# Kernel tuning notes

Hardware: AMD Instinct MI355X
Metric: run time of the kernel (lower is better)

## Reference

```python
import jax, jax.numpy as jnp
import numpy as np

B, T, H, A, E, V = 32, 128, 1024, 1024, 512, 512  # A==H required by the module's cat/Linear shapes


def setup_inputs() -> dict:
    key = jax.random.key(0)
    ks = jax.random.split(key, 13)
    s = 0.02
    return {
        "encoder_outputs": jax.random.normal(ks[0], (B, A, E), jnp.float32),
        "hidden": jax.random.normal(ks[1], (1, B, H), jnp.float32),
        "target_seq": jax.random.normal(ks[2], (B, T, H), jnp.float32),
        "W_att": jax.random.normal(ks[3], (H + A, A), jnp.float32) * s,
        "b_att": jax.random.normal(ks[4], (A,), jnp.float32) * s,
        "W_comb": jax.random.normal(ks[5], (H + E, H), jnp.float32) * s,
        "b_comb": jax.random.normal(ks[6], (H,), jnp.float32) * s,
        "W_ih": jax.random.normal(ks[7], (3 * H, H), jnp.float32) * s,
        "b_ih": jax.random.normal(ks[8], (3 * H,), jnp.float32) * s,
        "W_hh": jax.random.normal(ks[9], (3 * H, H), jnp.float32) * s,
        "b_hh": jax.random.normal(ks[10], (3 * H,), jnp.float32) * s,
        "W_out": jax.random.normal(ks[11], (H, V), jnp.float32) * s,
        "b_out": jax.random.normal(ks[12], (V,), jnp.float32) * s,
    }


def reference(encoder_outputs, hidden, target_seq, W_att, b_att, W_comb, b_comb,
              W_ih, b_ih, W_hh, b_hh, W_out, b_out):
    # Teacher forcing: decoder input at step t is zeros (t=0) then target_seq[:, t-1]
    dec_in = jnp.concatenate([jnp.zeros_like(target_seq[:, :1]), target_seq[:, :-1]], axis=1)  # [B,T,H]
    dec_ts = jnp.swapaxes(dec_in, 0, 1)  # [T,B,H]

    def step(h, dec):  # h: [B,H], dec: [B,H]
        # attention over encoder positions (softmax width A == encoder seq len)
        attn = jax.nn.softmax(jnp.concatenate([dec, h], axis=1) @ W_att + b_att, axis=1)  # [B,A]
        ctx = jnp.einsum('bl,ble->be', attn, encoder_outputs)  # [B,E]
        g = jax.nn.relu(jnp.concatenate([dec, ctx], axis=1) @ W_comb + b_comb)  # [B,H]
        # GRU cell (torch gate order r, z, n)
        gi = g @ W_ih.T + b_ih
        gh = h @ W_hh.T + b_hh
        ir, iz, i_n = jnp.split(gi, 3, axis=1)
        hr, hz, h_n = jnp.split(gh, 3, axis=1)
        r = jax.nn.sigmoid(ir + hr)
        z = jax.nn.sigmoid(iz + hz)
        n = jnp.tanh(i_n + r * h_n)
        h_new = (1.0 - z) * n + z * h
        out_tok = h_new @ W_out + b_out  # [B,V]
        return h_new, out_tok

    h_last, outs = jax.lax.scan(step, hidden[0], dec_ts)  # outs: [T,B,V]
    output_seq = jnp.swapaxes(outs, 0, 1)  # [B,T,V]
    return output_seq, h_last[None]
```

## Files before the change

kernel.cpp:

```cpp
#include <hip/hip_runtime.h>

typedef unsigned short u16;
typedef unsigned int u32;
typedef unsigned long long u64;
typedef short v8s __attribute__((ext_vector_type(8)));
typedef float v4f __attribute__((ext_vector_type(4)));

#define MFMA16(a, b, c) __builtin_amdgcn_mfma_f32_16x16x32_bf16((a), (b), (c), 0, 0, 0)

#define B_ 32
#define T_ 128
#define H_ 1024
#define A_ 1024
#define E_ 512
#define V_ 512
#define NBLK 256
#define NTH 512
#define NSLOT 32
#define ENC_LDS_BYTES 131072
#define SCRATCH_BYTES 28672
#define DSMEM_BYTES (ENC_LDS_BYTES + SCRATCH_BYTES)

__device__ __forceinline__ float b2f(u16 u) {
  union { u32 u; float f; } c; c.u = ((u32)u) << 16; return c.f;
}
__device__ __forceinline__ u16 f2b(float f) {
  union { float f; u32 u; } c; c.f = f;
  u32 x = c.u;
  x += 0x7fffu + ((x >> 16) & 1u);
  return (u16)(x >> 16);
}

__device__ __forceinline__ u32 ato_ld(const u32* p) {
  return __hip_atomic_load(p, __ATOMIC_RELAXED, __HIP_MEMORY_SCOPE_AGENT);
}
__device__ __forceinline__ void ato_st(u32* p, u32 v) {
  __hip_atomic_store(p, v, __ATOMIC_RELAXED, __HIP_MEMORY_SCOPE_AGENT);
}
__device__ __forceinline__ float ato_ldf(const float* p) {
  union { u32 u; float f; } c; c.u = ato_ld((const u32*)p); return c.f;
}
__device__ __forceinline__ void ato_stf(float* p, float v) {
  union { float f; u32 u; } c; c.f = v; ato_st((u32*)p, c.u);
}
__device__ __forceinline__ v8s ld_frag(const u16* p) {
  u64 a = __hip_atomic_load((const u64*)p, __ATOMIC_RELAXED, __HIP_MEMORY_SCOPE_AGENT);
  u64 b = __hip_atomic_load((const u64*)(p + 4), __ATOMIC_RELAXED, __HIP_MEMORY_SCOPE_AGENT);
  union { u64 q[2]; v8s v; } u; u.q[0] = a; u.q[1] = b; return u.v;
}

__device__ __forceinline__ void grid_bar(u32* arr, u32 ep) {
  asm volatile("s_waitcnt vmcnt(0)" ::: "memory");
  __syncthreads();
  u32* gen = arr + NBLK * NSLOT;
  if (blockIdx.x == 0) {
    int i = threadIdx.x;
    if (i >= 1 && i < NBLK) {
      while (__hip_atomic_load(arr + i * NSLOT, __ATOMIC_RELAXED, __HIP_MEMORY_SCOPE_AGENT) < ep)
        __builtin_amdgcn_s_sleep(1);
    }
    __syncthreads();
    if (threadIdx.x == 0)
      __hip_atomic_store(gen, ep, __ATOMIC_RELAXED, __HIP_MEMORY_SCOPE_AGENT);
  } else {
    if (threadIdx.x == 0) {
      __hip_atomic_store(arr + blockIdx.x * NSLOT, ep, __ATOMIC_RELAXED, __HIP_MEMORY_SCOPE_AGENT);
      while (__hip_atomic_load(gen, __ATOMIC_RELAXED, __HIP_MEMORY_SCOPE_AGENT) < ep)
        __builtin_amdgcn_s_sleep(1);
    }
    __syncthreads();
  }
  asm volatile("" ::: "memory");
}

__device__ __forceinline__ void gemm_nk(const u16* ah, const u16* al, size_t mstr,
                                        const u16* bp, int nk, v4f& c0, v4f& c1) {
  #pragma unroll 2
  for (int i = 0; i < nk; ++i) {
    v8s b   = *(const v8s*)(bp);
    v8s a0h = *(const v8s*)(ah);
    v8s a1h = *(const v8s*)(ah + mstr);
    v8s a0l = *(const v8s*)(al);
    v8s a1l = *(const v8s*)(al + mstr);
    c0 = MFMA16(a0h, b, c0);
    c1 = MFMA16(a1h, b, c1);
    c0 = MFMA16(a0l, b, c0);
    c1 = MFMA16(a1l, b, c1);
    ah += 32; al += 32; bp += 32;
  }
}
__device__ __forceinline__ void gemm_nk_a(const u16* ah, const u16* al, size_t mstr,
                                          const u16* bp, int nk, v4f& c0, v4f& c1) {
  #pragma unroll 2
  for (int i = 0; i < nk; ++i) {
    v8s b   = *(const v8s*)(bp);
    v8s a0h = ld_frag(ah);
    v8s a1h = ld_frag(ah + mstr);
    v8s a0l = ld_frag(al);
    v8s a1l = ld_frag(al + mstr);
    c0 = MFMA16(a0h, b, c0);
    c1 = MFMA16(a1h, b, c1);
    c0 = MFMA16(a0l, b, c0);
    c1 = MFMA16(a1l, b, c1);
    ah += 32; al += 32; bp += 32;
  }
}

__device__ __forceinline__ void red_store2(float* part, int wv, int lane, v4f c0, v4f c1) {
  float* p = part + (wv * 64 + lane) * 8;
  #pragma unroll
  for (int r = 0; r < 4; ++r) { p[r] = c0[r]; p[4 + r] = c1[r]; }
}
__device__ __forceinline__ float red_sum2(const float* part, int o) {
  int m = o >> 4, n = o & 15;
  int lane = (((m & 15) >> 2) << 4) + n;
  int idx = ((m >> 4) << 2) + (m & 3);
  float s = 0.f;
  #pragma unroll
  for (int w = 0; w < 8; ++w) s += part[(w * 64 + lane) * 8 + idx];
  return s;
}

__global__ void __launch_bounds__(NTH, 1)
dec_persist(const u16* __restrict__ tgt_hi, const u16* __restrict__ tgt_lo,
            const u16* __restrict__ WattT, const u16* __restrict__ Whh_b,
            const u16* __restrict__ Wih_b, const u16* __restrict__ WcombT,
            const float* __restrict__ enc_f,
            const float* __restrict__ batt, const float* __restrict__ bcomb,
            const float* __restrict__ bih, const float* __restrict__ bhh,
            float* h, float* logit, float* gh, float* g_dec, float* logit_dec,
            u16* ctx_hi, u16* ctx_lo, u16* g_hi, u16* g_lo,
            u16* hbf_hi, u16* hbf_lo, u16* hseqb, u32* bar)
{
  const int tid = threadIdx.x;
  const int bid = blockIdx.x;
  const int lane = tid & 63;
  const int wv = tid >> 6;
  const int ln = lane & 15;
  const int kq8 = (lane >> 4) * 8;

  extern __shared__ __align__(16) unsigned char dsm[];
  u16* lds_enc = (u16*)dsm;
  float* scratch = (float*)(dsm + ENC_LDS_BYTES);

  {
    int b = bid >> 3, e0 = (bid & 7) * 64;
    const float* src = enc_f + (size_t)b * A_ * E_ + e0 + (tid & 7) * 8;
    int seg = (tid & 7) * 8;
    for (int i = 0; i < 16; ++i) {
      int row = i * 64 + (tid >> 3);
      const float* sp = src + (size_t)row * E_;
      float4 a = *(const float4*)sp;
      float4 bq = *(const float4*)(sp + 4);
      u16 tmp[8] = {f2b(a.x), f2b(a.y), f2b(a.z), f2b(a.w),
                    f2b(bq.x), f2b(bq.y), f2b(bq.z), f2b(bq.w)};
      *(v8s*)(lds_enc + row * 64 + seg) = *(v8s*)tmp;
    }
  }

  u32 ep = 0;

  for (int t = 0; t < T_; ++t) {
    {
      float* part = scratch;
      int u = bid;
      v4f c0 = {0.f, 0.f, 0.f, 0.f}, c1 = {0.f, 0.f, 0.f, 0.f};
      if (u < 64) {
        int n0 = u * 16;
        const u16* bp = WattT + (size_t)(n0 + ln) * 2048 + 1024 + wv * 128 + kq8;
        size_t abase = (size_t)ln * H_ + wv * 128 + kq8;
        gemm_nk_a(hbf_hi + abase, hbf_lo + abase, (size_t)16 * H_, bp, 4, c0, c1);
      } else {
        int j0 = (u - 64) * 16;
        const u16* bp = Whh_b + (size_t)(j0 + ln) * H_ + wv * 128 + kq8;
        size_t abase = (size_t)ln * H_ + wv * 128 + kq8;
        gemm_nk_a(hbf_hi + abase, hbf_lo + abase, (size_t)16 * H_, bp, 4, c0, c1);
      }
      red_store2(part, wv, lane, c0, c1);
      __syncthreads();
      {
        float s = red_sum2(part, tid);
        int m = tid >> 4, n = tid & 15;
        if (u < 64) {
          int n0 = u * 16;
          float v = s + ato_ldf(&logit_dec[(t & 1) * (B_ * A_) + m * A_ + n0 + n])
                  + batt[n0 + n];
          ato_stf(&logit[m * A_ + n0 + n], v);
        } else {
          int j0 = (u - 64) * 16;
          ato_stf(&gh[(size_t)(j0 + n) * 32 + m], s + bhh[j0 + n]);
        }
      }
    }
    grid_bar(bar, ++ep);

    {
      float* p    = scratch;
      float* part = scratch + 1024;
      float* red  = scratch + 5120;
      float* sctx = scratch + 5136;
      int b = bid >> 3, e0 = (bid & 7) * 64;
      float v1 = ato_ldf(&logit[b * A_ + tid]);
      float v2 = ato_ldf(&logit[b * A_ + 512 + tid]);
      float mx = fmaxf(v1, v2);
      #pragma unroll
      for (int off = 32; off; off >>= 1) mx = fmaxf(mx, __shfl_xor(mx, off));
      if (lane == 0) red[wv] = mx;
      __syncthreads();
      float mfull = red[0];
      #pragma unroll
      for (int q = 1; q < 8; ++q) mfull = fmaxf(mfull, red[q]);
      float e1 = __expf(v1 - mfull), e2 = __expf(v2 - mfull);
      p[tid] = e1; p[512 + tid] = e2;
      float sm = e1 + e2;
      #pragma unroll
      for (int off = 32; off; off >>= 1) sm += __shfl_xor(sm, off);
      if (lane == 0) red[8 + wv] = sm;
      __syncthreads();
      float ssum = red[8];
      #pragma unroll
      for (int q = 1; q < 8; ++q) ssum += red[8 + q];
      float inv = 1.f / ssum;

      int le = lane & 7, lr = lane >> 3;
      float acc[8] = {0.f, 0.f, 0.f, 0.f, 0.f, 0.f, 0.f, 0.f};
      #pragma unroll 4
      for (int i = 0; i < 16; ++i) {
        int l = i * 64 + wv * 8 + lr;
        v8s w = *(const v8s*)(lds_enc + l * 64 + le * 8);
        float pv = p[l];
        #pragma unroll
        for (int r = 0; r < 8; ++r) acc[r] += pv * b2f((u16)w[r]);
      }
      float* pp = part + ((wv * 8 + lr) * 8 + le) * 8;
      #pragma unroll
      for (int r = 0; r < 8; ++r) pp[r] = acc[r];
      __syncthreads();
      if (tid < 64) {
        int eo = tid >> 3, r = tid & 7;
        float s = 0.f;
        #pragma unroll
        for (int q = 0; q < 64; ++q) s += part[q * 64 + eo * 8 + r];
        sctx[tid] = s * inv;
      }
      __syncthreads();
      if (tid < 32) {
        float s0 = sctx[2 * tid], s1 = sctx[2 * tid + 1];
        u16 h0 = f2b(s0), h1 = f2b(s1);
        u16 l0 = f2b(s0 - b2f(h0)), l1 = f2b(s1 - b2f(h1));
        int idx = b * E_ + e0 + 2 * tid;
        ato_st((u32*)(ctx_hi + idx), (u32)h0 | ((u32)h1 << 16));
        ato_st((u32*)(ctx_lo + idx), (u32)l0 | ((u32)l1 << 16));
      }
    }
    grid_bar(bar, ++ep);

    {
      if (bid < 64) {
        float* part = scratch;
        int n0 = bid * 16;
        v4f c0 = {0.f, 0.f, 0.f, 0.f}, c1 = {0.f, 0.f, 0.f, 0.f};
        const u16* bp = WcombT + (size_t)(n0 + ln) * 1536 + 1024 + wv * 64 + kq8;
        size_t abase = (size_t)ln * E_ + wv * 64 + kq8;
        gemm_nk_a(ctx_hi + abase, ctx_lo + abase, (size_t)16 * E_, bp, 2, c0, c1);
        red_store2(part, wv, lane, c0, c1);
        __syncthreads();
        int m = tid >> 4, n = tid & 15;
        float s = red_sum2(part, tid) + ato_ldf(&g_dec[(t & 1) * (B_ * H_) + m * H_ + n0 + n])
                + bcomb[n0 + n];
        s = fmaxf(s, 0.f);
        __syncthreads();
        float* gx = part;
        gx[m * 16 + n] = s;
        __syncthreads();
        if (tid < 256) {
          int m2 = tid >> 3, n2 = (tid & 7) * 2;
          float s0 = gx[m2 * 16 + n2], s1 = gx[m2 * 16 + n2 + 1];
          u16 h0 = f2b(s0), h1 = f2b(s1);
          u16 l0 = f2b(s0 - b2f(h0)), l1 = f2b(s1 - b2f(h1));
          int idx = m2 * H_ + n0 + n2;
          ato_st((u32*)(g_hi + idx), (u32)h0 | ((u32)h1 << 16));
          ato_st((u32*)(g_lo + idx), (u32)l0 | ((u32)l1 << 16));
        }
      }
    }
    grid_bar(bar, ++ep);

    {
      if (bid < 64) {
        float* part = scratch;
        float* hx   = scratch + 6144;
        int j0 = bid * 16;
        v4f c00 = {0.f,0.f,0.f,0.f}, c01 = c00, c02 = c00, c10 = c00, c11 = c00, c12 = c00;
        size_t abase = (size_t)ln * H_ + wv * 128 + kq8;
        const u16* ah = g_hi + abase;
        const u16* al = g_lo + abase;
        const u16* bp0 = Wih_b + (size_t)(j0 + ln) * H_ + wv * 128 + kq8;
        const u16* bp1 = bp0 + (size_t)H_ * H_;
        const u16* bp2 = bp0 + (size_t)2 * H_ * H_;
        #pragma unroll
        for (int i = 0; i < 4; ++i) {
          v8s b0 = *(const v8s*)bp0, b1 = *(const v8s*)bp1, b2 = *(const v8s*)bp2;
          v8s a0h = ld_frag(ah), a0l = ld_frag(al);
          v8s a1h = ld_frag(ah + 16 * H_), a1l = ld_frag(al + 16 * H_);
          c00 = MFMA16(a0h, b0, c00); c00 = MFMA16(a0l, b0, c00);
          c01 = MFMA16(a0h, b1, c01); c01 = MFMA16(a0l, b1, c01);
          c02 = MFMA16(a0h, b2, c02); c02 = MFMA16(a0l, b2, c02);
          c10 = MFMA16(a1h, b0, c10); c10 = MFMA16(a1l, b0, c10);
          c11 = MFMA16(a1h, b1, c11); c11 = MFMA16(a1l, b1, c11);
          c12 = MFMA16(a1h, b2, c12); c12 = MFMA16(a1l, b2, c12);
          ah += 32; al += 32; bp0 += 32; bp1 += 32; bp2 += 32;
        }
        #pragma unroll
        for (int pass = 0; pass < 2; ++pass) {
          float* pp = part + (wv * 64 + lane) * 12;
          if (pass == 0) {
            #pragma unroll
            for (int r = 0; r < 4; ++r) { pp[r] = c00[r]; pp[4 + r] = c01[r]; pp[8 + r] = c02[r]; }
          } else {
            #pragma unroll
            for (int r = 0; r < 4; ++r) { pp[r] = c10[r]; pp[4 + r] = c11[r]; pp[8 + r] = c12[r]; }
          }
          __syncthreads();
          if (tid < 256) {
            int obl = tid >> 4, jj = tid & 15;
            int ob = pass * 16 + obl;
            int j = j0 + jj;
            int lanei = ((obl >> 2) << 4) + jj;
            int rg = obl & 3;
            float ir = 0.f, iz = 0.f, in_ = 0.f;
            #pragma unroll
            for (int w = 0; w < 8; ++w) {
              const float* q = part + (w * 64 + lanei) * 12;
              ir += q[rg]; iz += q[4 + rg]; in_ += q[8 + rg];
            }
            ir += bih[j]; iz += bih[H_ + j]; in_ += bih[2 * H_ + j];
            float hr = ato_ldf(&gh[(size_t)j * 32 + ob]);
            float hz = ato_ldf(&gh[(size_t)(H_ + j) * 32 + ob]);
            float hn = ato_ldf(&gh[(size_t)(2 * H_ + j) * 32 + ob]);
            float r = 1.f / (1.f + __expf(-(ir + hr)));
            float z = 1.f / (1.f + __expf(-(iz + hz)));
            float n = tanhf(in_ + r * hn);
            float ho = h[ob * H_ + j];
            float hnew = (1.f - z) * n + z * ho;
            h[ob * H_ + j] = hnew;
            hx[ob * 16 + jj] = hnew;
          }
          __syncthreads();
        }
        if (tid < 256) {
          int ob2 = tid >> 3, j2 = (tid & 7) * 2;
          float v0 = hx[ob2 * 16 + j2], v1 = hx[ob2 * 16 + j2 + 1];
          u16 h0 = f2b(v0), h1 = f2b(v1);
          u16 l0 = f2b(v0 - b2f(h0)), l1 = f2b(v1 - b2f(h1));
          int idx = ob2 * H_ + j0 + j2;
          u32 hp = (u32)h0 | ((u32)h1 << 16);
          ato_st((u32*)(hbf_hi + idx), hp);
          ato_st((u32*)(hbf_lo + idx), (u32)l0 | ((u32)l1 << 16));
          *(u32*)(hseqb + ((size_t)t * 32 + ob2) * H_ + j0 + j2) = hp;
        }
      } else if (bid < 128) {
        if (t < T_ - 1) {
          float* part = scratch;
          int n0 = (bid - 64) * 16;
          v4f c0 = {0.f, 0.f, 0.f, 0.f}, c1 = {0.f, 0.f, 0.f, 0.f};
          size_t abase = ((size_t)ln * T_ + t) * H_ + wv * 128 + kq8;
          const u16* bp = WattT + (size_t)(n0 + ln) * 2048 + wv * 128 + kq8;
          gemm_nk(tgt_hi + abase, tgt_lo + abase, (size_t)16 * T_ * H_, bp, 4, c0, c1);
          red_store2(part, wv, lane, c0, c1);
          __syncthreads();
          int m = tid >> 4, n = tid & 15;
          ato_stf(&logit_dec[((t + 1) & 1) * (B_ * A_) + m * A_ + n0 + n], red_sum2(part, tid));
        }
      } else if (bid < 192) {
        if (t < T_ - 1) {
          float* part = scratch;
          int n0 = (bid - 128) * 16;
          v4f c0 = {0.f, 0.f, 0.f, 0.f}, c1 = {0.f, 0.f, 0.f, 0.f};
          size_t abase = ((size_t)ln * T_ + t) * H_ + wv * 128 + kq8;
          const u16* bp = WcombT + (size_t)(n0 + ln) * 1536 + wv * 128 + kq8;
          gemm_nk(tgt_hi + abase, tgt_lo + abase, (size_t)16 * T_ * H_, bp, 4, c0, c1);
          red_store2(part, wv, lane, c0, c1);
          __syncthreads();
          int m = tid >> 4, n = tid & 15;
          ato_stf(&g_dec[((t + 1) & 1) * (B_ * H_) + m * H_ + n0 + n], red_sum2(part, tid));
        }
      }
    }
    grid_bar(bar, ++ep);
  }
}

__global__ void __launch_bounds__(256, 2)
out_gemm(const u16* __restrict__ hseqb, const u16* __restrict__ WoutT,
         const float* __restrict__ bout, float* __restrict__ out)
{
  int tid = threadIdx.x, lane = tid & 63, wv = tid >> 6;
  int ln = lane & 15, kq8 = (lane >> 4) * 8;
  int m0 = (blockIdx.x >> 3) * 32;
  int n0 = (blockIdx.x & 7) * 64 + wv * 16;
  v4f c0 = {0.f, 0.f, 0.f, 0.f}, c1 = {0.f, 0.f, 0.f, 0.f};
  const u16* ap = hseqb + (size_t)(m0 + ln) * 1024 + kq8;
  const u16* bp = WoutT + (size_t)(n0 + ln) * 1024 + kq8;
  for (int i = 0; i < 32; ++i) {
    v8s b = *(const v8s*)bp;
    v8s a0 = *(const v8s*)ap;
    v8s a1 = *(const v8s*)(ap + 16 * 1024);
    c0 = MFMA16(a0, b, c0);
    c1 = MFMA16(a1, b, c1);
    ap += 32; bp += 32;
  }
  int v = n0 + ln;
  float bo = bout[v];
  int rbase = (lane >> 4) * 4;
  #pragma unroll
  for (int rg = 0; rg < 4; ++rg) {
    int m = m0 + rbase + rg;
    out[((size_t)(m & 31) * T_ + (m >> 5)) * V_ + v] = c0[rg] + bo;
    int m2 = m + 16;
    out[((size_t)(m2 & 31) * T_ + (m2 >> 5)) * V_ + v] = c1[rg] + bo;
  }
}

__global__ void __launch_bounds__(256)
hlast_copy(const float* __restrict__ h, float* __restrict__ out)
{
  int i = blockIdx.x * 256 + threadIdx.x;
  if (i < B_ * H_) out[(size_t)B_ * T_ * V_ + i] = h[i];
}

__global__ void __launch_bounds__(256)
k_cvt(const float* __restrict__ in, u16* __restrict__ out, int n)
{
  int stride = gridDim.x * 256;
  for (int i = blockIdx.x * 256 + threadIdx.x; i < n; i += stride) out[i] = f2b(in[i]);
}

__global__ void __launch_bounds__(256)
k_cvt_split(const float* __restrict__ in, u16* __restrict__ hi, u16* __restrict__ lo, int n)
{
  int stride = gridDim.x * 256;
  for (int i = blockIdx.x * 256 + threadIdx.x; i < n; i += stride) {
    float x = in[i];
    u16 a = f2b(x);
    hi[i] = a;
    lo[i] = f2b(x - b2f(a));
  }
}

__global__ void __launch_bounds__(256)
k_tr(const float* __restrict__ in, u16* __restrict__ out, int R, int C)
{
  __shared__ float tile[32][33];
  int tc = C >> 5;
  int r0 = (blockIdx.x / tc) << 5, c0 = (blockIdx.x % tc) << 5;
  int tx = threadIdx.x & 31, ty = threadIdx.x >> 5;
  #pragma unroll
  for (int q = 0; q < 4; ++q) {
    int r = ty + q * 8;
    tile[r][tx] = in[(size_t)(r0 + r) * C + c0 + tx];
  }
  __syncthreads();
  #pragma unroll
  for (int q = 0; q < 4; ++q) {
    int r = ty + q * 8;
    out[(size_t)(c0 + r) * R + r0 + tx] = f2b(tile[tx][r]);
  }
}

__global__ void __launch_bounds__(256)
k_init(const float* __restrict__ hidden, float* h, u16* hhi, u16* hlo)
{
  int i = blockIdx.x * 256 + threadIdx.x;
  if (i < B_ * H_) {
    float x = hidden[i];
    h[i] = x;
    u16 a = f2b(x);
    hhi[i] = a;
    hlo[i] = f2b(x - b2f(a));
  }
}

extern "C" void kernel_launch(void* const* d_in, const int* in_sizes, int n_in,
                              void* d_out, int out_size, void* d_ws, size_t ws_size,
                              hipStream_t stream) {
  (void)in_sizes; (void)n_in; (void)out_size; (void)ws_size;
  const float* enc    = (const float*)d_in[0];
  const float* hidden = (const float*)d_in[1];
  const float* tgt    = (const float*)d_in[2];
  const float* Watt   = (const float*)d_in[3];
  const float* batt   = (const float*)d_in[4];
  const float* Wcomb  = (const float*)d_in[5];
  const float* bcomb  = (const float*)d_in[6];
  const float* Wih    = (const float*)d_in[7];
  const float* bih    = (const float*)d_in[8];
  const float* Whh    = (const float*)d_in[9];
  const float* bhh    = (const float*)d_in[10];
  const float* Wout   = (const float*)d_in[11];
  const float* bout   = (const float*)d_in[12];

  size_t off = 0;
  char* base = (char*)d_ws;
  auto alloc = [&](size_t bytes) -> void* {
    void* p = base + off;
    off += (bytes + 255) & ~(size_t)255;
    return p;
  };
  size_t bar_bytes = (size_t)(NBLK * NSLOT + NSLOT) * 4;
  u32*   bar    = (u32*)  alloc(bar_bytes);
  float* h      = (float*)alloc(B_ * H_ * 4);
  float* logit  = (float*)alloc(B_ * A_ * 4);
  float* gh     = (float*)alloc((size_t)3 * H_ * B_ * 4);
  float* g_dec  = (float*)alloc((size_t)2 * B_ * H_ * 4);
  float* logit_dec = (float*)alloc((size_t)2 * B_ * A_ * 4);
  u16*   ctx_hi = (u16*)  alloc(B_ * E_ * 2);
  u16*   ctx_lo = (u16*)  alloc(B_ * E_ * 2);
  u16*   g_hi   = (u16*)  alloc(B_ * H_ * 2);
  u16*   g_lo   = (u16*)  alloc(B_ * H_ * 2);
  u16*   hbf_hi = (u16*)  alloc(B_ * H_ * 2);
  u16*   hbf_lo = (u16*)  alloc(B_ * H_ * 2);
  u16*   hseqb  = (u16*)  alloc((size_t)T_ * B_ * H_ * 2);
  u16*   tgt_hi = (u16*)  alloc((size_t)B_ * T_ * H_ * 2);
  u16*   tgt_lo = (u16*)  alloc((size_t)B_ * T_ * H_ * 2);
  u16*   WattT  = (u16*)  alloc((size_t)2048 * 1024 * 2);
  u16*   Whh_b  = (u16*)  alloc((size_t)3 * H_ * H_ * 2);
  u16*   Wih_b  = (u16*)  alloc((size_t)3 * H_ * H_ * 2);
  u16*   WcombT = (u16*)  alloc((size_t)1024 * 1536 * 2);
  u16*   WoutT  = (u16*)  alloc((size_t)512 * 1024 * 2);

  hipMemsetAsync(bar, 0, bar_bytes, stream);
  hipMemsetAsync(g_dec, 0, (size_t)2 * B_ * H_ * 4, stream);
  hipMemsetAsync(logit_dec, 0, (size_t)2 * B_ * A_ * 4, stream);

  k_cvt_split<<<2048, 256, 0, stream>>>(tgt, tgt_hi, tgt_lo, B_ * T_ * H_);
  k_cvt<<<2048, 256, 0, stream>>>(Whh, Whh_b, 3 * H_ * H_);
  k_cvt<<<2048, 256, 0, stream>>>(Wih, Wih_b, 3 * H_ * H_);
  k_tr<<<64 * 32, 256, 0, stream>>>(Watt, WattT, 2048, 1024);
  k_tr<<<48 * 32, 256, 0, stream>>>(Wcomb, WcombT, 1536, 1024);
  k_tr<<<32 * 16, 256, 0, stream>>>(Wout, WoutT, 1024, 512);
  k_init<<<128, 256, 0, stream>>>(hidden, h, hbf_hi, hbf_lo);

  hipFuncSetAttribute((const void*)dec_persist,
                      hipFuncAttributeMaxDynamicSharedMemorySize, DSMEM_BYTES);

  dec_persist<<<NBLK, NTH, DSMEM_BYTES, stream>>>(tgt_hi, tgt_lo, WattT, Whh_b, Wih_b, WcombT,
                                                  enc, batt, bcomb, bih, bhh,
                                                  h, logit, gh, g_dec, logit_dec,
                                                  ctx_hi, ctx_lo, g_hi, g_lo,
                                                  hbf_hi, hbf_lo, hseqb, bar);
  out_gemm<<<1024, 256, 0, stream>>>(hseqb, WoutT, bout, (float*)d_out);
  hlast_copy<<<128, 256, 0, stream>>>(h, (float*)d_out);
}
```

Before: 4.524 ms.

## Fuse ctx-to-comb projection into attention phase via atomic accumulation, drop a grid barrier

Each attention block now multiplies its 64-element context slice by the matching rows of the ctx part of W_comb and atomically adds the partial result into a float g accumulator. The separate comb GEMM phase and its grid barrier are removed, so there is one fewer global synchronization per timestep. The GRU input phase applies bias and ReLU and does the bf16 hi/lo split on the fly when loading g. The cost is fp32 atomics to global memory with nondeterministic summation order, extra zeroing stores for the double buffer, and a CUDA-core dot product in place of MFMA.

```diff
diff --git a/kernel.cpp b/kernel.cpp
--- a/kernel.cpp
+++ b/kernel.cpp
@@ -43,10 +43,30 @@
 __device__ __forceinline__ void ato_stf(float* p, float v) {
   union { float f; u32 u; } c; c.f = v; ato_st((u32*)p, c.u);
 }
+__device__ __forceinline__ void ato_addf(float* p, float v) {
+  __hip_atomic_fetch_add(p, v, __ATOMIC_RELAXED, __HIP_MEMORY_SCOPE_AGENT);
+}
 __device__ __forceinline__ v8s ld_frag(const u16* p) {
   u64 a = __hip_atomic_load((const u64*)p, __ATOMIC_RELAXED, __HIP_MEMORY_SCOPE_AGENT);
   u64 b = __hip_atomic_load((const u64*)(p + 4), __ATOMIC_RELAXED, __HIP_MEMORY_SCOPE_AGENT);
   union { u64 q[2]; v8s v; } u; u.q[0] = a; u.q[1] = b; return u.v;
+}
+__device__ __forceinline__ void ld_g8(const float* gp, const float* bc, v8s& hi, v8s& lo) {
+  float v[8];
+  #pragma unroll
+  for (int i = 0; i < 8; i += 2) {
+    u64 q = __hip_atomic_load((const u64*)(gp + i), __ATOMIC_RELAXED, __HIP_MEMORY_SCOPE_AGENT);
+    union { u64 q; float f[2]; } c; c.q = q;
+    v[i] = c.f[0]; v[i + 1] = c.f[1];
+  }
+  u16 hh[8], ll[8];
+  #pragma unroll
+  for (int i = 0; i < 8; ++i) {
+    float x = fmaxf(v[i] + bc[i], 0.f);
+    u16 a = f2b(x);
+    hh[i] = a; ll[i] = f2b(x - b2f(a));
+  }
+  hi = *(v8s*)hh; lo = *(v8s*)ll;
 }
 
 __device__ __forceinline__ void grid_bar(u32* arr, u32 ep) {
@@ -125,11 +145,11 @@
 dec_persist(const u16* __restrict__ tgt_hi, const u16* __restrict__ tgt_lo,
             const u16* __restrict__ WattT, const u16* __restrict__ Whh_b,
             const u16* __restrict__ Wih_b, const u16* __restrict__ WcombT,
+            const u16* __restrict__ Wc_ctx,
             const float* __restrict__ enc_f,
             const float* __restrict__ batt, const float* __restrict__ bcomb,
             const float* __restrict__ bih, const float* __restrict__ bhh,
-            float* h, float* logit, float* gh, float* g_dec, float* logit_dec,
-            u16* ctx_hi, u16* ctx_lo, u16* g_hi, u16* g_lo,
+            float* h, float* logit, float* gh, float* g_acc, float* logit_dec,
             u16* hbf_hi, u16* hbf_lo, u16* hseqb, u32* bar)
 {
   const int tid = threadIdx.x;
@@ -163,15 +183,15 @@
   for (int t = 0; t < T_; ++t) {
     {
       float* part = scratch;
-      int u = bid;
       v4f c0 = {0.f, 0.f, 0.f, 0.f}, c1 = {0.f, 0.f, 0.f, 0.f};
-      if (u < 64) {
-        int n0 = u * 16;
+      if (bid < 64) {
+        ato_stf(&g_acc[((t + 1) & 1) * (B_ * H_) + bid * 512 + tid], 0.f);
+        int n0 = bid * 16;
         const u16* bp = WattT + (size_t)(n0 + ln) * 2048 + 1024 + wv * 128 + kq8;
         size_t abase = (size_t)ln * H_ + wv * 128 + kq8;
         gemm_nk_a(hbf_hi + abase, hbf_lo + abase, (size_t)16 * H_, bp, 4, c0, c1);
       } else {
-        int j0 = (u - 64) * 16;
+        int j0 = (bid - 64) * 16;
         const u16* bp = Whh_b + (size_t)(j0 + ln) * H_ + wv * 128 + kq8;
         size_t abase = (size_t)ln * H_ + wv * 128 + kq8;
         gemm_nk_a(hbf_hi + abase, hbf_lo + abase, (size_t)16 * H_, bp, 4, c0, c1);
@@ -181,13 +201,13 @@
       {
         float s = red_sum2(part, tid);
         int m = tid >> 4, n = tid & 15;
-        if (u < 64) {
-          int n0 = u * 16;
+        if (bid < 64) {
+          int n0 = bid * 16;
           float v = s + ato_ldf(&logit_dec[(t & 1) * (B_ * A_) + m * A_ + n0 + n])
                   + batt[n0 + n];
           ato_stf(&logit[m * A_ + n0 + n], v);
         } else {
-          int j0 = (u - 64) * 16;
+          int j0 = (bid - 64) * 16;
           ato_stf(&gh[(size_t)(j0 + n) * 32 + m], s + bhh[j0 + n]);
         }
       }
@@ -199,7 +219,7 @@
       float* part = scratch + 1024;
       float* red  = scratch + 5120;
       float* sctx = scratch + 5136;
-      int b = bid >> 3, e0 = (bid & 7) * 64;
+      int b = bid >> 3, es = bid & 7;
       float v1 = ato_ldf(&logit[b * A_ + tid]);
       float v2 = ato_ldf(&logit[b * A_ + 512 + tid]);
       float mx = fmaxf(v1, v2);
@@ -244,44 +264,19 @@
         sctx[tid] = s * inv;
       }
       __syncthreads();
-      if (tid < 32) {
-        float s0 = sctx[2 * tid], s1 = sctx[2 * tid + 1];
-        u16 h0 = f2b(s0), h1 = f2b(s1);
-        u16 l0 = f2b(s0 - b2f(h0)), l1 = f2b(s1 - b2f(h1));
-        int idx = b * E_ + e0 + 2 * tid;
-        ato_st((u32*)(ctx_hi + idx), (u32)h0 | ((u32)h1 << 16));
-        ato_st((u32*)(ctx_lo + idx), (u32)l0 | ((u32)l1 << 16));
-      }
-    }
-    grid_bar(bar, ++ep);
-
-    {
-      if (bid < 64) {
-        float* part = scratch;
-        int n0 = bid * 16;
-        v4f c0 = {0.f, 0.f, 0.f, 0.f}, c1 = {0.f, 0.f, 0.f, 0.f};
-        const u16* bp = WcombT + (size_t)(n0 + ln) * 1536 + 1024 + wv * 64 + kq8;
-        size_t abase = (size_t)ln * E_ + wv * 64 + kq8;
-        gemm_nk_a(ctx_hi + abase, ctx_lo + abase, (size_t)16 * E_, bp, 2, c0, c1);
-        red_store2(part, wv, lane, c0, c1);
-        __syncthreads();
-        int m = tid >> 4, n = tid & 15;
-        float s = red_sum2(part, tid) + ato_ldf(&g_dec[(t & 1) * (B_ * H_) + m * H_ + n0 + n])
-                + bcomb[n0 + n];
-        s = fmaxf(s, 0.f);
-        __syncthreads();
-        float* gx = part;
-        gx[m * 16 + n] = s;
-        __syncthreads();
-        if (tid < 256) {
-          int m2 = tid >> 3, n2 = (tid & 7) * 2;
-          float s0 = gx[m2 * 16 + n2], s1 = gx[m2 * 16 + n2 + 1];
-          u16 h0 = f2b(s0), h1 = f2b(s1);
-          u16 l0 = f2b(s0 - b2f(h0)), l1 = f2b(s1 - b2f(h1));
-          int idx = m2 * H_ + n0 + n2;
-          ato_st((u32*)(g_hi + idx), (u32)h0 | ((u32)h1 << 16));
-          ato_st((u32*)(g_lo + idx), (u32)l0 | ((u32)l1 << 16));
-        }
+      {
+        const u16* wrow = Wc_ctx + (size_t)(es * 64) * H_ + tid * 2;
+        float a0 = 0.f, a1 = 0.f;
+        #pragma unroll 4
+        for (int e = 0; e < 64; ++e) {
+          u32 w = *(const u32*)(wrow + (size_t)e * H_);
+          float pv = sctx[e];
+          a0 += pv * b2f((u16)w);
+          a1 += pv * b2f((u16)(w >> 16));
+        }
+        float* gp = g_acc + (t & 1) * (B_ * H_) + b * H_ + tid * 2;
+        ato_addf(gp, a0);
+        ato_addf(gp + 1, a1);
       }
     }
     grid_bar(bar, ++ep);
@@ -292,24 +287,24 @@
         float* hx   = scratch + 6144;
         int j0 = bid * 16;
         v4f c00 = {0.f,0.f,0.f,0.f}, c01 = c00, c02 = c00, c10 = c00, c11 = c00, c12 = c00;
-        size_t abase = (size_t)ln * H_ + wv * 128 + kq8;
-        const u16* ah = g_hi + abase;
-        const u16* al = g_lo + abase;
-        const u16* bp0 = Wih_b + (size_t)(j0 + ln) * H_ + wv * 128 + kq8;
+        const float* gbase = g_acc + (t & 1) * (B_ * H_);
+        int koff = wv * 128 + kq8;
+        const u16* bp0 = Wih_b + (size_t)(j0 + ln) * H_ + koff;
         const u16* bp1 = bp0 + (size_t)H_ * H_;
         const u16* bp2 = bp0 + (size_t)2 * H_ * H_;
         #pragma unroll
         for (int i = 0; i < 4; ++i) {
           v8s b0 = *(const v8s*)bp0, b1 = *(const v8s*)bp1, b2 = *(const v8s*)bp2;
-          v8s a0h = ld_frag(ah), a0l = ld_frag(al);
-          v8s a1h = ld_frag(ah + 16 * H_), a1l = ld_frag(al + 16 * H_);
+          v8s a0h, a0l, a1h, a1l;
+          ld_g8(gbase + (size_t)ln * H_ + koff, bcomb + koff, a0h, a0l);
+          ld_g8(gbase + (size_t)(ln + 16) * H_ + koff, bcomb + koff, a1h, a1l);
           c00 = MFMA16(a0h, b0, c00); c00 = MFMA16(a0l, b0, c00);
           c01 = MFMA16(a0h, b1, c01); c01 = MFMA16(a0l, b1, c01);
           c02 = MFMA16(a0h, b2, c02); c02 = MFMA16(a0l, b2, c02);
           c10 = MFMA16(a1h, b0, c10); c10 = MFMA16(a1l, b0, c10);
           c11 = MFMA16(a1h, b1, c11); c11 = MFMA16(a1l, b1, c11);
           c12 = MFMA16(a1h, b2, c12); c12 = MFMA16(a1l, b2, c12);
-          ah += 32; al += 32; bp0 += 32; bp1 += 32; bp2 += 32;
+          koff += 32; bp0 += 32; bp1 += 32; bp2 += 32;
         }
         #pragma unroll
         for (int pass = 0; pass < 2; ++pass) {
@@ -383,7 +378,7 @@
           red_store2(part, wv, lane, c0, c1);
           __syncthreads();
           int m = tid >> 4, n = tid & 15;
-          ato_stf(&g_dec[((t + 1) & 1) * (B_ * H_) + m * H_ + n0 + n], red_sum2(part, tid));
+          ato_addf(&g_acc[((t + 1) & 1) * (B_ * H_) + m * H_ + n0 + n], red_sum2(part, tid));
         }
       }
     }
@@ -511,12 +506,8 @@
   float* h      = (float*)alloc(B_ * H_ * 4);
   float* logit  = (float*)alloc(B_ * A_ * 4);
   float* gh     = (float*)alloc((size_t)3 * H_ * B_ * 4);
-  float* g_dec  = (float*)alloc((size_t)2 * B_ * H_ * 4);
+  float* g_acc  = (float*)alloc((size_t)2 * B_ * H_ * 4);
   float* logit_dec = (float*)alloc((size_t)2 * B_ * A_ * 4);
-  u16*   ctx_hi = (u16*)  alloc(B_ * E_ * 2);
-  u16*   ctx_lo = (u16*)  alloc(B_ * E_ * 2);
-  u16*   g_hi   = (u16*)  alloc(B_ * H_ * 2);
-  u16*   g_lo   = (u16*)  alloc(B_ * H_ * 2);
   u16*   hbf_hi = (u16*)  alloc(B_ * H_ * 2);
   u16*   hbf_lo = (u16*)  alloc(B_ * H_ * 2);
   u16*   hseqb  = (u16*)  alloc((size_t)T_ * B_ * H_ * 2);
@@ -526,15 +517,17 @@
   u16*   Whh_b  = (u16*)  alloc((size_t)3 * H_ * H_ * 2);
   u16*   Wih_b  = (u16*)  alloc((size_t)3 * H_ * H_ * 2);
   u16*   WcombT = (u16*)  alloc((size_t)1024 * 1536 * 2);
+  u16*   Wc_ctx = (u16*)  alloc((size_t)512 * 1024 * 2);
   u16*   WoutT  = (u16*)  alloc((size_t)512 * 1024 * 2);
 
   hipMemsetAsync(bar, 0, bar_bytes, stream);
-  hipMemsetAsync(g_dec, 0, (size_t)2 * B_ * H_ * 4, stream);
+  hipMemsetAsync(g_acc, 0, (size_t)2 * B_ * H_ * 4, stream);
   hipMemsetAsync(logit_dec, 0, (size_t)2 * B_ * A_ * 4, stream);
 
   k_cvt_split<<<2048, 256, 0, stream>>>(tgt, tgt_hi, tgt_lo, B_ * T_ * H_);
   k_cvt<<<2048, 256, 0, stream>>>(Whh, Whh_b, 3 * H_ * H_);
   k_cvt<<<2048, 256, 0, stream>>>(Wih, Wih_b, 3 * H_ * H_);
+  k_cvt<<<2048, 256, 0, stream>>>(Wcomb + (size_t)1024 * H_, Wc_ctx, 512 * H_);
   k_tr<<<64 * 32, 256, 0, stream>>>(Watt, WattT, 2048, 1024);
   k_tr<<<48 * 32, 256, 0, stream>>>(Wcomb, WcombT, 1536, 1024);
   k_tr<<<32 * 16, 256, 0, stream>>>(Wout, WoutT, 1024, 512);
@@ -543,10 +536,10 @@
   hipFuncSetAttribute((const void*)dec_persist,
                       hipFuncAttributeMaxDynamicSharedMemorySize, DSMEM_BYTES);
 
-  dec_persist<<<NBLK, NTH, DSMEM_BYTES, stream>>>(tgt_hi, tgt_lo, WattT, Whh_b, Wih_b, WcombT,
-                                                  enc, batt, bcomb, bih, bhh,
-                                                  h, logit, gh, g_dec, logit_dec,
-                                                  ctx_hi, ctx_lo, g_hi, g_lo,
+  dec_persist<<<NBLK, NTH, DSMEM_BYTES, stream>>>(tgt_hi, tgt_lo, WattT, Whh_b, Wih_b,
+                                                  WcombT, Wc_ctx, enc,
+                                                  batt, bcomb, bih, bhh,
+                                                  h, logit, gh, g_acc, logit_dec,
                                                   hbf_hi, hbf_lo, hseqb, bar);
   out_gemm<<<1024, 256, 0, stream>>>(hseqb, WoutT, bout, (float*)d_out);
   hlast_copy<<<128, 256, 0, stream>>>(h, (float*)d_out);
```

Measured after the change: 4.399 ms. -2.8%, faster.
